# Optimization experiments

Measured on AMD Instinct MI355X. Metric: run time of the kernel, lower is better.

## Reference

```python
import jax, jax.numpy as jnp
import numpy as np
from jax import lax

N, L, D, P, H, QK, VP = 1, 512, 256, 128, 8, 8, 8
FIN = H * P + H * VP * 7 + H * 7  # 1528: pair + value-point + beta features


def _l2g(R, t, p):
    # local_to_global: q = R @ p + t, applied over flattened point dims
    s = p.shape
    p3 = p.reshape(s[0], s[1], -1, 3)
    q = jnp.einsum('nlij,nlmj->nlmi', R, p3) + t[:, :, None, :]
    return q.reshape(s)


def _g2l(R, t, q):
    # global_to_local: p = R^T @ (q - t)
    s = q.shape
    q3 = q.reshape(s[0], s[1], -1, 3)
    p = jnp.einsum('nlji,nlmj->nlmi', R, q3 - t[:, :, None, :])
    return p.reshape(s)


def _inorm(x):  # InstanceNorm2d, affine=False, eps=1e-5, NCHW
    m = x.mean(axis=(2, 3), keepdims=True)
    v = x.var(axis=(2, 3), keepdims=True)
    return (x - m) * lax.rsqrt(v + 1e-5)


def _conv3(x, w, b):  # 3x3, stride 1, pad 1
    y = lax.conv_general_dilated(x, w, (1, 1), [(1, 1), (1, 1)],
                                 dimension_numbers=('NCHW', 'OIHW', 'NCHW'))
    return y + b[None, :, None, None]


def _ln(x, g, b):  # LayerNorm over last dim, eps=1e-5
    m = x.mean(-1, keepdims=True)
    v = x.var(-1, keepdims=True)
    return (x - m) * lax.rsqrt(v + 1e-5) * g + b


def _leaky(x):  # LeakyReLU, negative_slope=0.01
    return jnp.where(x >= 0, x, 0.01 * x)


def setup_inputs():
    key = jax.random.key(0)
    ks = jax.random.split(key, 24)
    s = 0.05
    return {
        'R': jax.random.normal(ks[0], (N, L, 3, 3), jnp.float32),
        't': jax.random.normal(ks[1], (N, L, 3), jnp.float32),
        'p_CB': jax.random.normal(ks[2], (N, L, 3), jnp.float32),
        'x': jax.random.normal(ks[3], (N, L, D), jnp.float32),
        'z': jax.random.normal(ks[4], (N, L, L, P), jnp.float32),
        'W_p2h': jax.random.normal(ks[5], (P, H), jnp.float32) * s,
        'gamma': jnp.ones((1, 1, H), jnp.float32),
        'Wq': jax.random.normal(ks[6], (D, H * QK * 3), jnp.float32) * s,
        'Wk': jax.random.normal(ks[7], (D, H * QK * 3), jnp.float32) * s,
        'Wv': jax.random.normal(ks[8], (D, H * VP * 3), jnp.float32) * s,
        'W1': jax.random.normal(ks[9], (FIN, 2 * D), jnp.float32) * s,
        'b1': jnp.zeros((2 * D,), jnp.float32),
        'ln1_g': jnp.ones((2 * D,), jnp.float32),
        'ln1_b': jnp.zeros((2 * D,), jnp.float32),
        'W2': jax.random.normal(ks[10], (2 * D, D), jnp.float32) * s,
        'b2': jnp.zeros((D,), jnp.float32),
        'ca_w': jax.random.normal(ks[11], (H, 2 * H, 3, 3), jnp.float32) * s,
        'ca_b': jnp.zeros((H,), jnp.float32),
        'ln_g': jnp.ones((D,), jnp.float32),
        'ln_b': jnp.zeros((D,), jnp.float32),
        'cp_w': jax.random.normal(ks[12], (P, H + P, 3, 3), jnp.float32) * s,
        'cp_b': jnp.zeros((P,), jnp.float32),
        'mask': jnp.ones((N, L), dtype=bool),
    }


def reference(R, t, p_CB, x, z, W_p2h, gamma, Wq, Wk, Wv, W1, b1, ln1_g, ln1_b,
              W2, b2, ca_w, ca_b, ln_g, ln_b, cp_w, cp_b, mask):
    n, l = x.shape[:2]
    # pair logits [n,l,l,H]
    logits_pair = jnp.einsum('nijp,ph->nijh', z, W_p2h)
    # spatial (point) logits: squared distances between global q/k points
    q_s = _l2g(R, t, (x @ Wq).reshape(n, l, H * QK, 3)).reshape(n, l, H, QK * 3)
    k_s = _l2g(R, t, (x @ Wk).reshape(n, l, H * QK, 3)).reshape(n, l, H, QK * 3)
    ssd = ((q_s ** 2).sum(-1)[:, :, None, :] + (k_s ** 2).sum(-1)[:, None, :, :]
           - 2.0 * jnp.einsum('nihd,njhd->nijh', q_s, k_s))
    logits_spatial = ssd * (-gamma * jnp.sqrt(2.0 / (9.0 * QK)) / 2.0)
    # conv2dalpha: InstanceNorm -> 3x3 conv -> LeakyReLU over the LxL grid
    lg = jnp.concatenate([logits_pair, logits_spatial], axis=-1).transpose(0, 3, 1, 2)
    logits_sum = _leaky(_conv3(_inorm(lg), ca_w, ca_b)).transpose(0, 2, 3, 1)
    mask_row = mask[:, :, None, None]
    mask_pair = mask_row & mask[:, None, :, None]
    logits_sum = jnp.where(mask_pair, logits_sum, logits_sum - 1e6)
    alpha = jax.nn.softmax(logits_sum, axis=2)
    alpha = jnp.where(mask_row, alpha, 0.0)
    # pair aggregation [n,l,H*P]
    feat_p2n = jnp.einsum('nijh,nijp->nihp', alpha, z).reshape(n, l, H * P)
    # spatial (value point) aggregation
    v_pts = _l2g(R, t, (x @ Wv).reshape(n, l, H, VP, 3))
    aggr = jnp.einsum('nijh,njhvc->nihvc', alpha, v_pts)
    fp = _g2l(R, t, aggr)  # [n,l,H,VP,3]
    fn = jnp.sqrt((fp ** 2).sum(-1))
    fdir = fp / (fn[..., None] + 1e-6)
    feat_spatial = jnp.concatenate(
        [fp.reshape(n, l, -1), fn.reshape(n, l, -1), fdir.reshape(n, l, -1)], -1)
    # beta (CB point) aggregation
    aggr_b = jnp.einsum('nijh,njc->nihc', alpha, p_CB)
    fpb = _g2l(R, t, aggr_b)  # [n,l,H,3]
    fnb = jnp.sqrt((fpb ** 2).sum(-1))
    fdb = fpb / (fnb[..., None] + 1e-6)
    feat_beta = jnp.concatenate([fpb.reshape(n, l, -1), fnb, fdb.reshape(n, l, -1)], -1)
    # out_transform: Linear -> LayerNorm -> LeakyReLU -> Linear
    feat_all = jnp.concatenate([feat_p2n, feat_spatial, feat_beta], -1)
    h1 = _leaky(_ln(feat_all @ W1 + b1, ln1_g, ln1_b))
    fa = h1 @ W2 + b2
    fa = jnp.where(mask[..., None], fa, 0.0)
    x_out = _ln(x + fa, ln_g, ln_b)
    # alpha2pair: InstanceNorm -> 3x3 conv -> LeakyReLU
    pz = jnp.concatenate([z, alpha], -1).transpose(0, 3, 1, 2)
    pair_out = _leaky(_conv3(_inorm(pz), cp_w, cp_b)).transpose(0, 2, 3, 1)
    return (x_out, pair_out)
```

## Files before the change

kernel.cpp:

```cpp
#include <hip/hip_runtime.h>
#include <hip/hip_bf16.h>
#include <math.h>

#define Lr 512
#define LL (512*512)

typedef __bf16 bf16x8 __attribute__((ext_vector_type(8)));
typedef float f32x16 __attribute__((ext_vector_type(16)));

static __device__ __forceinline__ unsigned short f2bf(float f) {
    union { float f; unsigned u; } a; a.f = f;
    unsigned r = a.u + 0x7fff + ((a.u >> 16) & 1);
    return (unsigned short)(r >> 16);
}

__global__ __launch_bounds__(512) void zero_stats_k(float* lg_acc, float* pz_acc) {
    int t = threadIdx.x;
    if (t < 32) lg_acc[t] = 0.f;
    if (t < 272) pz_acc[t] = 0.f;
}

__global__ __launch_bounds__(256) void wb_prep_k(const float* __restrict__ cpw, unsigned short* __restrict__ wb) {
    int idx = blockIdx.x * 256 + threadIdx.x;
    if (idx >= 128 * 1296) return;
    int o = idx / 1296, k = idx % 1296;
    int tap = k / 144, c = k % 144;
    float v = (c < 136) ? cpw[(o * 136 + c) * 9 + tap] : 0.f;
    wb[idx] = f2bf(v);
}

__device__ __forceinline__ const float* qkv_colptr(const float* Wq, const float* Wk, const float* Wv, int c) {
    return c < 192 ? (Wq + c) : (c < 384 ? (Wk + c - 192) : (Wv + c - 384));
}

__global__ __launch_bounds__(256) void qkv_k(const float* __restrict__ x,
        const float* __restrict__ Wq, const float* __restrict__ Wk, const float* __restrict__ Wv,
        const float* __restrict__ R, const float* __restrict__ tv,
        float* __restrict__ qs, float* __restrict__ ks, float* __restrict__ vp,
        float* __restrict__ q2, float* __restrict__ k2) {
    __shared__ float xrow[256];
    __shared__ float praw[576];
    __shared__ float tr[576];
    __shared__ float Rt[12];
    int i = blockIdx.x, t = threadIdx.x;
    xrow[t] = x[i * 256 + t];
    if (t < 12) Rt[t] = (t < 9) ? R[i * 9 + t] : tv[i * 3 + t - 9];
    __syncthreads();
    const float* p0 = qkv_colptr(Wq, Wk, Wv, t);
    const float* p1 = qkv_colptr(Wq, Wk, Wv, t + 256);
    const float* p2 = qkv_colptr(Wq, Wk, Wv, t < 64 ? t + 512 : 575);
    float a0 = 0.f, a1 = 0.f, a2 = 0.f;
    for (int f = 0; f < 256; f++) {
        float xv = xrow[f];
        a0 += xv * p0[f * 192];
        a1 += xv * p1[f * 192];
        a2 += xv * p2[f * 192];
    }
    praw[t] = a0; praw[t + 256] = a1;
    if (t < 64) praw[t + 512] = a2;
    __syncthreads();
    if (t < 192) {
        int seg = t / 64, pt = t % 64;
        float b0 = praw[seg * 192 + pt * 3], b1_ = praw[seg * 192 + pt * 3 + 1], b2_ = praw[seg * 192 + pt * 3 + 2];
        #pragma unroll
        for (int r = 0; r < 3; r++)
            tr[seg * 192 + pt * 3 + r] = Rt[r * 3] * b0 + Rt[r * 3 + 1] * b1_ + Rt[r * 3 + 2] * b2_ + Rt[9 + r];
    }
    __syncthreads();
    if (t < 8) {
        float s = 0.f;
        #pragma unroll
        for (int d = 0; d < 24; d++) { float v = tr[t * 24 + d]; s += v * v; }
        q2[i * 8 + t] = s;
    } else if (t < 16) {
        int h = t - 8; float s = 0.f;
        #pragma unroll
        for (int d = 0; d < 24; d++) { float v = tr[192 + h * 24 + d]; s += v * v; }
        k2[i * 8 + h] = s;
    }
    for (int f = t; f < 576; f += 256) {
        float v = tr[f];
        if (f < 192) qs[i * 192 + f] = v;
        else if (f < 384) ks[i * 192 + f - 192] = v;
        else vp[i * 192 + f - 384] = v;
    }
}

__global__ __launch_bounds__(256) void zstats_k(const float4* __restrict__ z4, float* pz_acc) {
    __shared__ float acc[256];
    int t = threadIdx.x;
    acc[t] = 0.f;
    __syncthreads();
    float s[4] = {0,0,0,0}, s2[4] = {0,0,0,0};
    size_t base = (size_t)blockIdx.x * 4096;
    #pragma unroll
    for (int k = 0; k < 16; k++) {
        float4 v = z4[base + k * 256 + t];
        s[0] += v.x; s2[0] += v.x * v.x;
        s[1] += v.y; s2[1] += v.y * v.y;
        s[2] += v.z; s2[2] += v.z * v.z;
        s[3] += v.w; s2[3] += v.w * v.w;
    }
    int c0 = (4 * t) & 127;
    #pragma unroll
    for (int u = 0; u < 4; u++) {
        atomicAdd(&acc[(c0 + u) * 2], s[u]);
        atomicAdd(&acc[(c0 + u) * 2 + 1], s2[u]);
    }
    __syncthreads();
    if (t < 128) {
        atomicAdd(&pz_acc[t * 2], acc[t * 2]);
        atomicAdd(&pz_acc[t * 2 + 1], acc[t * 2 + 1]);
    }
}

__global__ __launch_bounds__(256) void lg_k(const float* __restrict__ z,
        const float* __restrict__ Wp2h, const float* __restrict__ gamma,
        const float* __restrict__ qs, const float* __restrict__ ks,
        const float* __restrict__ q2, const float* __restrict__ k2,
        float* __restrict__ lg, float* lg_acc) {
    __shared__ float zl[32 * 132];
    __shared__ float wh[8 * 132];
    __shared__ float qrow[192];
    __shared__ float q2row[8];
    __shared__ float sacc[32];
    int i = blockIdx.x, t = threadIdx.x;
    for (int f = t; f < 1024; f += 256) { int h = f >> 7, p = f & 127; wh[h * 132 + p] = Wp2h[p * 8 + h]; }
    if (t < 192) qrow[t] = qs[i * 192 + t];
    if (t < 8) q2row[t] = q2[i * 8 + t];
    if (t < 32) sacc[t] = 0.f;
    int jl = t >> 3, h = t & 7;
    float gsc = -gamma[h] * 0.08333333333333333f;
    float sp = 0.f, sp2 = 0.f, ss = 0.f, ss2 = 0.f;
    __syncthreads();
    for (int jt = 0; jt < 16; jt++) {
        int j0 = jt * 32;
        const float4* zsrc = (const float4*)(z + (size_t)(i * 512 + j0) * 128);
        #pragma unroll
        for (int r = 0; r < 4; r++) {
            int idx4 = r * 256 + t;
            int zjl = idx4 >> 5, p4 = idx4 & 31;
            *(float4*)&zl[zjl * 132 + p4 * 4] = zsrc[idx4];
        }
        __syncthreads();
        int j = j0 + jl;
        float accp = 0.f;
        const float4* za = (const float4*)&zl[jl * 132];
        const float4* wa = (const float4*)&wh[h * 132];
        #pragma unroll
        for (int p4 = 0; p4 < 32; p4++) {
            float4 a = za[p4], b = wa[p4];
            accp += a.x * b.x + a.y * b.y + a.z * b.z + a.w * b.w;
        }
        const float4* kp = (const float4*)(ks + (size_t)j * 192 + h * 24);
        const float4* qp = (const float4*)&qrow[h * 24];
        float dqk = 0.f;
        #pragma unroll
        for (int d4 = 0; d4 < 6; d4++) {
            float4 a = qp[d4], b = kp[d4];
            dqk += a.x * b.x + a.y * b.y + a.z * b.z + a.w * b.w;
        }
        float ssd = q2row[h] + k2[j * 8 + h] - 2.f * dqk;
        float lgs = ssd * gsc;
        lg[(size_t)h * LL + i * 512 + j] = accp;
        lg[(size_t)(8 + h) * LL + i * 512 + j] = lgs;
        sp += accp; sp2 += accp * accp; ss += lgs; ss2 += lgs * lgs;
        __syncthreads();
    }
    atomicAdd(&sacc[h * 2], sp);        atomicAdd(&sacc[h * 2 + 1], sp2);
    atomicAdd(&sacc[16 + h * 2], ss);   atomicAdd(&sacc[16 + h * 2 + 1], ss2);
    __syncthreads();
    if (t < 16) {
        atomicAdd(&lg_acc[t * 2], sacc[t * 2]);
        atomicAdd(&lg_acc[t * 2 + 1], sacc[t * 2 + 1]);
    }
}

__global__ void finalize_k(const float* __restrict__ acc, float* __restrict__ mr, int nch, float npix) {
    int t = threadIdx.x;
    if (t < nch) {
        float m = acc[t * 2] / npix;
        float v = acc[t * 2 + 1] / npix - m * m;
        mr[t * 2] = m;
        mr[t * 2 + 1] = rsqrtf(fmaxf(v, 0.f) + 1e-5f);
    }
}

__global__ __launch_bounds__(256) void ca_softmax_k(const float* __restrict__ lg,
        const float* __restrict__ lgmr, const float* __restrict__ caw, const float* __restrict__ cab,
        float* __restrict__ alpha, float* pz_acc) {
    __shared__ float wl[1152];
    __shared__ float mr[32];
    __shared__ float cb[8];
    __shared__ float red[64];
    int i = blockIdx.x, t = threadIdx.x;
    for (int f = t; f < 1152; f += 256) {
        int o = f & 7, k = f >> 3; int c = k / 9, r = k % 9;
        wl[f] = caw[(o * 16 + c) * 9 + r];
    }
    if (t < 32) mr[t] = lgmr[t];
    if (t < 8) cb[t] = cab[t];
    __syncthreads();
    float acc0[8], acc1[8];
    #pragma unroll
    for (int o = 0; o < 8; o++) { acc0[o] = 0.f; acc1[o] = 0.f; }
    int j0 = t, j1 = t + 256;
    const float4* w4 = (const float4*)wl;
    for (int c = 0; c < 16; c++) {
        float m = mr[c * 2], rs = mr[c * 2 + 1];
        const float* lgc = lg + (size_t)c * LL;
        #pragma unroll
        for (int di = 0; di < 3; di++) {
            int row = i - 1 + di;
            if (row < 0 || row >= 512) continue;
            const float* lr = lgc + (size_t)row * 512;
            float v0[3], v1[3];
            v0[0] = (j0 > 0) ? (lr[j0 - 1] - m) * rs : 0.f;
            v0[1] = (lr[j0] - m) * rs;
            v0[2] = (lr[j0 + 1] - m) * rs;
            v1[0] = (lr[j1 - 1] - m) * rs;
            v1[1] = (lr[j1] - m) * rs;
            v1[2] = (j1 < 511) ? (lr[j1 + 1] - m) * rs : 0.f;
            int wb = (c * 9 + di * 3) * 2;
            #pragma unroll
            for (int dj = 0; dj < 3; dj++) {
                float4 wa = w4[wb + dj * 2], wbv = w4[wb + dj * 2 + 1];
                acc0[0] += wa.x * v0[dj]; acc0[1] += wa.y * v0[dj]; acc0[2] += wa.z * v0[dj]; acc0[3] += wa.w * v0[dj];
                acc0[4] += wbv.x * v0[dj]; acc0[5] += wbv.y * v0[dj]; acc0[6] += wbv.z * v0[dj]; acc0[7] += wbv.w * v0[dj];
                acc1[0] += wa.x * v1[dj]; acc1[1] += wa.y * v1[dj]; acc1[2] += wa.z * v1[dj]; acc1[3] += wa.w * v1[dj];
                acc1[4] += wbv.x * v1[dj]; acc1[5] += wbv.y * v1[dj]; acc1[6] += wbv.z * v1[dj]; acc1[7] += wbv.w * v1[dj];
            }
        }
    }
    float s0[8], s1[8];
    #pragma unroll
    for (int o = 0; o < 8; o++) {
        float v = acc0[o] + cb[o]; s0[o] = v >= 0.f ? v : 0.01f * v;
        float w = acc1[o] + cb[o]; s1[o] = w >= 0.f ? w : 0.01f * w;
    }
    int lane = t & 63, wid = t >> 6;
    float mx[8];
    #pragma unroll
    for (int o = 0; o < 8; o++) mx[o] = fmaxf(s0[o], s1[o]);
    for (int off = 1; off < 64; off <<= 1) {
        #pragma unroll
        for (int o = 0; o < 8; o++) mx[o] = fmaxf(mx[o], __shfl_xor(mx[o], off));
    }
    if (lane == 0) {
        #pragma unroll
        for (int o = 0; o < 8; o++) red[wid * 8 + o] = mx[o];
    }
    __syncthreads();
    float M[8];
    #pragma unroll
    for (int o = 0; o < 8; o++) M[o] = fmaxf(fmaxf(red[o], red[8 + o]), fmaxf(red[16 + o], red[24 + o]));
    float e0[8], e1[8], sm[8];
    #pragma unroll
    for (int o = 0; o < 8; o++) { e0[o] = expf(s0[o] - M[o]); e1[o] = expf(s1[o] - M[o]); sm[o] = e0[o] + e1[o]; }
    __syncthreads();
    for (int off = 1; off < 64; off <<= 1) {
        #pragma unroll
        for (int o = 0; o < 8; o++) sm[o] += __shfl_xor(sm[o], off);
    }
    if (lane == 0) {
        #pragma unroll
        for (int o = 0; o < 8; o++) red[wid * 8 + o] = sm[o];
    }
    __syncthreads();
    float a0[8], a1[8], st_s[8], st_q[8];
    #pragma unroll
    for (int o = 0; o < 8; o++) {
        float rden = 1.f / (red[o] + red[8 + o] + red[16 + o] + red[24 + o]);
        a0[o] = e0[o] * rden; a1[o] = e1[o] * rden;
        st_s[o] = a0[o] + a1[o];
        st_q[o] = a0[o] * a0[o] + a1[o] * a1[o];
    }
    size_t base = (size_t)i * 512;
    #pragma unroll
    for (int o = 0; o < 8; o++) {
        alpha[(size_t)o * LL + base + t] = a0[o];
        alpha[(size_t)o * LL + base + t + 256] = a1[o];
    }
    __syncthreads();
    for (int off = 1; off < 64; off <<= 1) {
        #pragma unroll
        for (int o = 0; o < 8; o++) { st_s[o] += __shfl_xor(st_s[o], off); st_q[o] += __shfl_xor(st_q[o], off); }
    }
    if (lane == 0) {
        #pragma unroll
        for (int o = 0; o < 8; o++) { red[wid * 8 + o] = st_s[o]; red[32 + wid * 8 + o] = st_q[o]; }
    }
    __syncthreads();
    if (t < 8) {
        float ts = red[t] + red[8 + t] + red[16 + t] + red[24 + t];
        float tq = red[32 + t] + red[40 + t] + red[48 + t] + red[56 + t];
        atomicAdd(&pz_acc[(128 + t) * 2], ts);
        atomicAdd(&pz_acc[(128 + t) * 2 + 1], tq);
    }
}

__global__ __launch_bounds__(256) void feat_mlp_k(
        const float* __restrict__ alpha, const float* __restrict__ z,
        const float* __restrict__ vp, const float* __restrict__ pcb,
        const float* __restrict__ R, const float* __restrict__ tv,
        const float* __restrict__ W1, const float* __restrict__ b1,
        const float* __restrict__ ln1g, const float* __restrict__ ln1b,
        const float* __restrict__ W2, const float* __restrict__ b2,
        const float* __restrict__ lng, const float* __restrict__ lnb,
        const float* __restrict__ x, float* __restrict__ xout) {
    __shared__ float al[8 * 512];
    __shared__ float zl[64 * 128];
    __shared__ float feat[1536];
    __shared__ float h1[512];
    __shared__ float agg[216];
    __shared__ float Rt[12];
    __shared__ float redl[8];
    int i = blockIdx.x, t = threadIdx.x;
    for (int f = t; f < 4096; f += 256) al[f] = alpha[(size_t)(f >> 9) * LL + i * 512 + (f & 511)];
    if (t < 12) Rt[t] = (t < 9) ? R[i * 9 + t] : tv[i * 3 + t - 9];
    __syncthreads();
    if (t < 216) {
        float a = 0.f;
        if (t < 192) {
            int h = t / 24;
            const float* vptr = vp + t;
            const float* ar = al + h * 512;
            for (int j = 0; j < 512; j++) a += ar[j] * vptr[(size_t)j * 192];
        } else {
            int u = t - 192; int h = u / 3, cc = u % 3;
            const float* ar = al + h * 512;
            for (int j = 0; j < 512; j++) a += ar[j] * pcb[j * 3 + cc];
        }
        agg[t] = a;
    }
    float4 accp = {0.f, 0.f, 0.f, 0.f};
    int hh = t >> 5, p4 = t & 31;
    for (int jc = 0; jc < 8; jc++) {
        const float4* zsrc = (const float4*)(z + (size_t)(i * 512 + jc * 64) * 128);
        #pragma unroll
        for (int r = 0; r < 8; r++) ((float4*)zl)[r * 256 + t] = zsrc[r * 256 + t];
        __syncthreads();
        const float* ar = al + hh * 512 + jc * 64;
        const float4* zv = (const float4*)zl + p4;
        #pragma unroll 4
        for (int jl = 0; jl < 64; jl++) {
            float a = ar[jl];
            float4 v = zv[jl * 32];
            accp.x += a * v.x; accp.y += a * v.y; accp.z += a * v.z; accp.w += a * v.w;
        }
        __syncthreads();
    }
    *(float4*)&feat[hh * 128 + p4 * 4] = accp;
    __syncthreads();
    if (t < 64) {
        int h = t >> 3, v = t & 7;
        float d0 = agg[h * 24 + v * 3] - Rt[9];
        float d1 = agg[h * 24 + v * 3 + 1] - Rt[10];
        float d2 = agg[h * 24 + v * 3 + 2] - Rt[11];
        float f0 = Rt[0] * d0 + Rt[3] * d1 + Rt[6] * d2;
        float f1 = Rt[1] * d0 + Rt[4] * d1 + Rt[7] * d2;
        float f2 = Rt[2] * d0 + Rt[5] * d1 + Rt[8] * d2;
        float n = sqrtf(f0 * f0 + f1 * f1 + f2 * f2);
        float rn = 1.f / (n + 1e-6f);
        feat[1024 + h * 24 + v * 3] = f0;
        feat[1024 + h * 24 + v * 3 + 1] = f1;
        feat[1024 + h * 24 + v * 3 + 2] = f2;
        feat[1216 + h * 8 + v] = n;
        feat[1280 + h * 24 + v * 3] = f0 * rn;
        feat[1280 + h * 24 + v * 3 + 1] = f1 * rn;
        feat[1280 + h * 24 + v * 3 + 2] = f2 * rn;
    } else if (t < 72) {
        int h = t - 64;
        float d0 = agg[192 + h * 3] - Rt[9];
        float d1 = agg[192 + h * 3 + 1] - Rt[10];
        float d2 = agg[192 + h * 3 + 2] - Rt[11];
        float f0 = Rt[0] * d0 + Rt[3] * d1 + Rt[6] * d2;
        float f1 = Rt[1] * d0 + Rt[4] * d1 + Rt[7] * d2;
        float f2 = Rt[2] * d0 + Rt[5] * d1 + Rt[8] * d2;
        float n = sqrtf(f0 * f0 + f1 * f1 + f2 * f2);
        float rn = 1.f / (n + 1e-6f);
        feat[1472 + h * 3] = f0; feat[1472 + h * 3 + 1] = f1; feat[1472 + h * 3 + 2] = f2;
        feat[1496 + h] = n;
        feat[1504 + h * 3] = f0 * rn; feat[1504 + h * 3 + 1] = f1 * rn; feat[1504 + h * 3 + 2] = f2 * rn;
    }
    __syncthreads();
    float acc0 = b1[t], acc1 = b1[t + 256];
    const float4* f4 = (const float4*)feat;
    for (int f = 0; f < 1528; f += 4) {
        float4 fv = f4[f >> 2];
        const float* w = W1 + (size_t)f * 512 + t;
        acc0 += fv.x * w[0] + fv.y * w[512] + fv.z * w[1024] + fv.w * w[1536];
        const float* w2p = w + 256;
        acc1 += fv.x * w2p[0] + fv.y * w2p[512] + fv.z * w2p[1024] + fv.w * w2p[1536];
    }
    int lane = t & 63, wid = t >> 6;
    float s = acc0 + acc1, s2 = acc0 * acc0 + acc1 * acc1;
    for (int off = 1; off < 64; off <<= 1) { s += __shfl_xor(s, off); s2 += __shfl_xor(s2, off); }
    if (lane == 0) { redl[wid * 2] = s; redl[wid * 2 + 1] = s2; }
    __syncthreads();
    float S = redl[0] + redl[2] + redl[4] + redl[6];
    float S2 = redl[1] + redl[3] + redl[5] + redl[7];
    float mean = S / 512.f;
    float rstd = rsqrtf(fmaxf(S2 / 512.f - mean * mean, 0.f) + 1e-5f);
    float hv0 = (acc0 - mean) * rstd * ln1g[t] + ln1b[t];
    float hv1 = (acc1 - mean) * rstd * ln1g[t + 256] + ln1b[t + 256];
    hv0 = hv0 >= 0.f ? hv0 : 0.01f * hv0;
    hv1 = hv1 >= 0.f ? hv1 : 0.01f * hv1;
    h1[t] = hv0; h1[t + 256] = hv1;
    __syncthreads();
    float a2 = b2[t];
    const float4* h14 = (const float4*)h1;
    for (int k = 0; k < 512; k += 4) {
        float4 hv = h14[k >> 2];
        const float* w = W2 + (size_t)k * 256 + t;
        a2 += hv.x * w[0] + hv.y * w[256] + hv.z * w[512] + hv.w * w[768];
    }
    float xv = x[i * 256 + t] + a2;
    float ss_ = xv, sq_ = xv * xv;
    for (int off = 1; off < 64; off <<= 1) { ss_ += __shfl_xor(ss_, off); sq_ += __shfl_xor(sq_, off); }
    __syncthreads();
    if (lane == 0) { redl[wid * 2] = ss_; redl[wid * 2 + 1] = sq_; }
    __syncthreads();
    float Sx = redl[0] + redl[2] + redl[4] + redl[6];
    float Sx2 = redl[1] + redl[3] + redl[5] + redl[7];
    float mx = Sx / 256.f;
    float rsx = rsqrtf(fmaxf(Sx2 / 256.f - mx * mx, 0.f) + 1e-5f);
    xout[i * 256 + t] = (xv - mx) * rsx * lng[t] + lnb[t];
}

__global__ __launch_bounds__(256) void conv_mfma_k(
        const float* __restrict__ z, const float* __restrict__ alpha,
        const float* __restrict__ pzmr, const unsigned short* __restrict__ wb,
        const float* __restrict__ cpb, float* __restrict__ pout) {
    __shared__ unsigned short rowbuf[130 * 144];
    __shared__ float mr[272];
    int t = threadIdx.x;
    int i  = blockIdx.x >> 2;
    int j0 = (blockIdx.x & 3) * 128;
    for (int f = t; f < 272; f += 256) mr[f] = pzmr[f];
    int w = t >> 6, lane = t & 63;
    int l31 = lane & 31, lhi = lane >> 5;
    int mt0 = (w & 1) * 64;
    int nt0 = (w >> 1) * 64;
    f32x16 acc00 = {}, acc01 = {}, acc10 = {}, acc11 = {};
    for (int di = 0; di < 3; di++) {
        int grow = i - 1 + di;
        bool rowok = (grow >= 0 && grow < 512);
        __syncthreads();
        for (int f4 = t; f4 < 130 * 34; f4 += 256) {
            int col = f4 / 34, c4 = (f4 % 34) * 4;
            int gcol = j0 - 1 + col;
            float4 v = {0.f, 0.f, 0.f, 0.f};
            if (rowok && gcol >= 0 && gcol < 512) {
                int sp = grow * 512 + gcol;
                if (c4 < 128) {
                    v = ((const float4*)z)[(size_t)sp * 32 + (c4 >> 2)];
                } else {
                    int h0 = c4 - 128;
                    v.x = alpha[(size_t)h0 * LL + sp];
                    v.y = alpha[(size_t)(h0 + 1) * LL + sp];
                    v.z = alpha[(size_t)(h0 + 2) * LL + sp];
                    v.w = alpha[(size_t)(h0 + 3) * LL + sp];
                }
                v.x = (v.x - mr[c4 * 2])     * mr[c4 * 2 + 1];
                v.y = (v.y - mr[c4 * 2 + 2]) * mr[c4 * 2 + 3];
                v.z = (v.z - mr[c4 * 2 + 4]) * mr[c4 * 2 + 5];
                v.w = (v.w - mr[c4 * 2 + 6]) * mr[c4 * 2 + 7];
            }
            ushort4 pk;
            pk.x = f2bf(v.x); pk.y = f2bf(v.y); pk.z = f2bf(v.z); pk.w = f2bf(v.w);
            *(ushort4*)&rowbuf[col * 144 + c4] = pk;
        }
        for (int f = t; f < 130 * 2; f += 256) {
            int col = f >> 1, g = f & 1;
            ushort4 zr = {0, 0, 0, 0};
            *(ushort4*)&rowbuf[col * 144 + 136 + g * 4] = zr;
        }
        __syncthreads();
        #pragma unroll
        for (int dj = 0; dj < 3; dj++) {
            int tap = di * 3 + dj;
            const unsigned short* wp0 = wb + (size_t)(nt0 + l31) * 1296 + tap * 144 + lhi * 8;
            const unsigned short* wp1 = wp0 + 32 * 1296;
            const unsigned short* ap0 = &rowbuf[(mt0 + l31 + dj) * 144 + lhi * 8];
            const unsigned short* ap1 = ap0 + 32 * 144;
            #pragma unroll
            for (int ks = 0; ks < 9; ks++) {
                bf16x8 a0 = *(const bf16x8*)(ap0 + ks * 16);
                bf16x8 a1 = *(const bf16x8*)(ap1 + ks * 16);
                bf16x8 b0 = *(const bf16x8*)(wp0 + ks * 16);
                bf16x8 b1 = *(const bf16x8*)(wp1 + ks * 16);
                acc00 = __builtin_amdgcn_mfma_f32_32x32x16_bf16(a0, b0, acc00, 0, 0, 0);
                acc01 = __builtin_amdgcn_mfma_f32_32x32x16_bf16(a0, b1, acc01, 0, 0, 0);
                acc10 = __builtin_amdgcn_mfma_f32_32x32x16_bf16(a1, b0, acc10, 0, 0, 0);
                acc11 = __builtin_amdgcn_mfma_f32_32x32x16_bf16(a1, b1, acc11, 0, 0, 0);
            }
        }
    }
    #pragma unroll
    for (int mi = 0; mi < 2; mi++) {
        #pragma unroll
        for (int ni = 0; ni < 2; ni++) {
            const f32x16* a = (mi == 0) ? (ni == 0 ? &acc00 : &acc01) : (ni == 0 ? &acc10 : &acc11);
            int nb = nt0 + ni * 32 + l31;
            float bias = cpb[nb];
            #pragma unroll
            for (int r = 0; r < 16; r++) {
                int m = mt0 + mi * 32 + 4 * lhi + (r & 3) + 8 * (r >> 2);
                float v = (*a)[r] + bias;
                v = v >= 0.f ? v : 0.01f * v;
                pout[((size_t)(i * 512 + j0 + m)) * 128 + nb] = v;
            }
        }
    }
}

extern "C" void kernel_launch(void* const* d_in, const int* in_sizes, int n_in,
                              void* d_out, int out_size, void* d_ws, size_t ws_size,
                              hipStream_t stream) {
    (void)in_sizes; (void)n_in; (void)out_size; (void)ws_size;
    const float* R    = (const float*)d_in[0];
    const float* tv   = (const float*)d_in[1];
    const float* pcb  = (const float*)d_in[2];
    const float* x    = (const float*)d_in[3];
    const float* z    = (const float*)d_in[4];
    const float* wp2h = (const float*)d_in[5];
    const float* gamma= (const float*)d_in[6];
    const float* Wq   = (const float*)d_in[7];
    const float* Wk   = (const float*)d_in[8];
    const float* Wv   = (const float*)d_in[9];
    const float* W1   = (const float*)d_in[10];
    const float* b1   = (const float*)d_in[11];
    const float* ln1g = (const float*)d_in[12];
    const float* ln1b = (const float*)d_in[13];
    const float* W2   = (const float*)d_in[14];
    const float* b2   = (const float*)d_in[15];
    const float* caw  = (const float*)d_in[16];
    const float* cab  = (const float*)d_in[17];
    const float* lng  = (const float*)d_in[18];
    const float* lnb  = (const float*)d_in[19];
    const float* cpw  = (const float*)d_in[20];
    const float* cpb  = (const float*)d_in[21];

    float* ws = (float*)d_ws;
    float* qs     = ws;
    float* ks     = qs + 98304;
    float* vp     = ks + 98304;
    float* q2     = vp + 98304;
    float* k2     = q2 + 4096;
    float* lg_acc = k2 + 4096;
    float* lg_mr  = lg_acc + 32;
    float* pz_acc = lg_mr + 32;
    float* pz_mr  = pz_acc + 272;
    unsigned short* wbq = (unsigned short*)(pz_mr + 272);
    float* lg     = pz_mr + 272 + 82944;
    float* alpha  = lg + 16 * LL;

    float* xout = (float*)d_out;
    float* pout = xout + 131072;

    hipLaunchKernelGGL(zero_stats_k, dim3(1), dim3(512), 0, stream, lg_acc, pz_acc);
    hipLaunchKernelGGL(wb_prep_k, dim3(648), dim3(256), 0, stream, cpw, wbq);
    hipLaunchKernelGGL(qkv_k, dim3(512), dim3(256), 0, stream, x, Wq, Wk, Wv, R, tv, qs, ks, vp, q2, k2);
    hipLaunchKernelGGL(zstats_k, dim3(2048), dim3(256), 0, stream, (const float4*)z, pz_acc);
    hipLaunchKernelGGL(lg_k, dim3(512), dim3(256), 0, stream, z, wp2h, gamma, qs, ks, q2, k2, lg, lg_acc);
    hipLaunchKernelGGL(finalize_k, dim3(1), dim3(64), 0, stream, lg_acc, lg_mr, 16, 262144.f);
    hipLaunchKernelGGL(ca_softmax_k, dim3(512), dim3(256), 0, stream, lg, lg_mr, caw, cab, alpha, pz_acc);
    hipLaunchKernelGGL(finalize_k, dim3(1), dim3(192), 0, stream, pz_acc, pz_mr, 136, 262144.f);
    hipLaunchKernelGGL(feat_mlp_k, dim3(512), dim3(256), 0, stream,
                       alpha, z, vp, pcb, R, tv, W1, b1, ln1g, ln1b, W2, b2, lng, lnb, x, xout);
    hipLaunchKernelGGL(conv_mfma_k, dim3(2048), dim3(256), 0, stream, z, alpha, pz_mr, wbq, cpb, pout);
}
```

Baseline: 799.0 us.

## Fold instance-norm into conv weights and pre-pack pair input as bf16

The instance-norm scale is folded into the bf16 conv weights. The mean shift becomes a per-output, per-tap bias correction, with explicit handling of image borders where zero padding drops taps. The z statistics pass and the softmax kernel now also write a pre-normalized bf16 copy of z and alpha in a channel-chunked layout. This lets the conv kernel load tiles with plain 16-byte copies instead of reading fp32 z/alpha, normalizing and converting on every 3x3 row reload. It also swizzles block order, and it adds an extra bf16 buffer write, a changed rounding point (raw values rather than normalized ones are quantized), and more workspace.

Result: faster. 782.1 us (-2.1%).

```diff
diff --git a/kernel.cpp b/kernel.cpp
--- a/kernel.cpp
+++ b/kernel.cpp
@@ -4,6 +4,7 @@
 
 #define Lr 512
 #define LL (512*512)
+#define PZROW 73728
 
 typedef __bf16 bf16x8 __attribute__((ext_vector_type(8)));
 typedef float f32x16 __attribute__((ext_vector_type(16)));
@@ -14,19 +15,35 @@
     return (unsigned short)(r >> 16);
 }
 
+static __device__ __forceinline__ unsigned pack2(float lo, float hi) {
+    return (unsigned)f2bf(lo) | ((unsigned)f2bf(hi) << 16);
+}
+
 __global__ __launch_bounds__(512) void zero_stats_k(float* lg_acc, float* pz_acc) {
     int t = threadIdx.x;
     if (t < 32) lg_acc[t] = 0.f;
     if (t < 272) pz_acc[t] = 0.f;
 }
 
-__global__ __launch_bounds__(256) void wb_prep_k(const float* __restrict__ cpw, unsigned short* __restrict__ wb) {
+__global__ __launch_bounds__(256) void wb_prep_k(const float* __restrict__ cpw,
+        const float* __restrict__ pzmr, unsigned short* __restrict__ wb) {
     int idx = blockIdx.x * 256 + threadIdx.x;
     if (idx >= 128 * 1296) return;
     int o = idx / 1296, k = idx % 1296;
     int tap = k / 144, c = k % 144;
-    float v = (c < 136) ? cpw[(o * 136 + c) * 9 + tap] : 0.f;
+    float v = (c < 136) ? cpw[(o * 136 + c) * 9 + tap] * pzmr[c * 2 + 1] : 0.f;
     wb[idx] = f2bf(v);
+}
+
+__global__ __launch_bounds__(128) void kc_prep_k(const float* __restrict__ cpw,
+        const float* __restrict__ pzmr, float* __restrict__ kc) {
+    int idx = blockIdx.x * 128 + threadIdx.x;
+    if (idx >= 1152) return;
+    int o = idx / 9, tap = idx % 9;
+    float s = 0.f;
+    for (int c = 0; c < 136; c++)
+        s += cpw[(o * 136 + c) * 9 + tap] * pzmr[c * 2 + 1] * pzmr[c * 2];
+    kc[idx] = -s;
 }
 
 __device__ __forceinline__ const float* qkv_colptr(const float* Wq, const float* Wk, const float* Wv, int c) {
@@ -86,26 +103,35 @@
     }
 }
 
-__global__ __launch_bounds__(256) void zstats_k(const float4* __restrict__ z4, float* pz_acc) {
+__global__ __launch_bounds__(256) void zstats_pzb_k(const float4* __restrict__ z4,
+        float* pz_acc, unsigned short* __restrict__ pzb) {
     __shared__ float acc[256];
     int t = threadIdx.x;
     acc[t] = 0.f;
     __syncthreads();
-    float s[4] = {0,0,0,0}, s2[4] = {0,0,0,0};
-    size_t base = (size_t)blockIdx.x * 4096;
-    #pragma unroll
-    for (int k = 0; k < 16; k++) {
-        float4 v = z4[base + k * 256 + t];
-        s[0] += v.x; s2[0] += v.x * v.x;
-        s[1] += v.y; s2[1] += v.y * v.y;
-        s[2] += v.z; s2[2] += v.z * v.z;
-        s[3] += v.w; s2[3] += v.w * v.w;
-    }
-    int c0 = (4 * t) & 127;
-    #pragma unroll
-    for (int u = 0; u < 4; u++) {
-        atomicAdd(&acc[(c0 + u) * 2], s[u]);
-        atomicAdd(&acc[(c0 + u) * 2 + 1], s2[u]);
+    int chunk = t & 15, pl = t >> 4;
+    int p0 = blockIdx.x * 128;
+    float s[8], s2[8];
+    #pragma unroll
+    for (int u = 0; u < 8; u++) { s[u] = 0.f; s2[u] = 0.f; }
+    #pragma unroll
+    for (int k = 0; k < 8; k++) {
+        int pos = p0 + k * 16 + pl;
+        const float4* src = z4 + (size_t)pos * 32 + chunk * 2;
+        float4 v0 = src[0], v1 = src[1];
+        float vv[8] = {v0.x, v0.y, v0.z, v0.w, v1.x, v1.y, v1.z, v1.w};
+        #pragma unroll
+        for (int u = 0; u < 8; u++) { s[u] += vv[u]; s2[u] += vv[u] * vv[u]; }
+        uint4 q;
+        q.x = pack2(vv[0], vv[1]); q.y = pack2(vv[2], vv[3]);
+        q.z = pack2(vv[4], vv[5]); q.w = pack2(vv[6], vv[7]);
+        int row = pos >> 9, col = pos & 511;
+        *(uint4*)(pzb + ((size_t)row * 18 + chunk) * 4096 + col * 8) = q;
+    }
+    #pragma unroll
+    for (int u = 0; u < 8; u++) {
+        atomicAdd(&acc[(chunk * 8 + u) * 2], s[u]);
+        atomicAdd(&acc[(chunk * 8 + u) * 2 + 1], s2[u]);
     }
     __syncthreads();
     if (t < 128) {
@@ -188,7 +214,7 @@
 
 __global__ __launch_bounds__(256) void ca_softmax_k(const float* __restrict__ lg,
         const float* __restrict__ lgmr, const float* __restrict__ caw, const float* __restrict__ cab,
-        float* __restrict__ alpha, float* pz_acc) {
+        float* __restrict__ alpha, float* pz_acc, unsigned short* __restrict__ pzb) {
     __shared__ float wl[1152];
     __shared__ float mr[32];
     __shared__ float cb[8];
@@ -280,6 +306,19 @@
     for (int o = 0; o < 8; o++) {
         alpha[(size_t)o * LL + base + t] = a0[o];
         alpha[(size_t)o * LL + base + t + 256] = a1[o];
+    }
+    {
+        uint4 p0, p1;
+        p0.x = pack2(a0[0], a0[1]); p0.y = pack2(a0[2], a0[3]);
+        p0.z = pack2(a0[4], a0[5]); p0.w = pack2(a0[6], a0[7]);
+        p1.x = pack2(a1[0], a1[1]); p1.y = pack2(a1[2], a1[3]);
+        p1.z = pack2(a1[4], a1[5]); p1.w = pack2(a1[6], a1[7]);
+        unsigned short* pb = pzb + (size_t)i * PZROW + 16 * 4096;
+        *(uint4*)(pb + (size_t)t * 8) = p0;
+        *(uint4*)(pb + (size_t)(t + 256) * 8) = p1;
+        uint4 zz = {0u, 0u, 0u, 0u};
+        *(uint4*)(pb + 4096 + (size_t)t * 8) = zz;
+        *(uint4*)(pb + 4096 + (size_t)(t + 256) * 8) = zz;
     }
     __syncthreads();
     for (int off = 1; off < 64; off <<= 1) {
@@ -429,15 +468,31 @@
 }
 
 __global__ __launch_bounds__(256) void conv_mfma_k(
-        const float* __restrict__ z, const float* __restrict__ alpha,
-        const float* __restrict__ pzmr, const unsigned short* __restrict__ wb,
-        const float* __restrict__ cpb, float* __restrict__ pout) {
-    __shared__ unsigned short rowbuf[130 * 144];
-    __shared__ float mr[272];
+        const unsigned short* __restrict__ pzb, const unsigned short* __restrict__ wb,
+        const float* __restrict__ kc, const float* __restrict__ cpb,
+        float* __restrict__ pout) {
+    __shared__ unsigned short abuf[2368 * 8];
+    __shared__ float csA[128];
+    __shared__ float cs0[128];
+    __shared__ float cs2[128];
     int t = threadIdx.x;
-    int i  = blockIdx.x >> 2;
-    int j0 = (blockIdx.x & 3) * 128;
-    for (int f = t; f < 272; f += 256) mr[f] = pzmr[f];
+    int bid = blockIdx.x;
+    int swz = (bid & 7) * 256 + (bid >> 3);
+    int i = swz >> 2;
+    int j0 = (swz & 3) * 128;
+    if (t < 128) {
+        int o = t;
+        float a0 = 0.f, a1 = 0.f, a2 = 0.f;
+        #pragma unroll
+        for (int di = 0; di < 3; di++) {
+            int grow = i - 1 + di;
+            if (grow < 0 || grow > 511) continue;
+            a0 += kc[o * 9 + di * 3];
+            a1 += kc[o * 9 + di * 3 + 1];
+            a2 += kc[o * 9 + di * 3 + 2];
+        }
+        cs0[o] = a0; cs2[o] = a2; csA[o] = cpb[o] + a0 + a1 + a2;
+    }
     int w = t >> 6, lane = t & 63;
     int l31 = lane & 31, lhi = lane >> 5;
     int mt0 = (w & 1) * 64;
@@ -447,34 +502,15 @@
         int grow = i - 1 + di;
         bool rowok = (grow >= 0 && grow < 512);
         __syncthreads();
-        for (int f4 = t; f4 < 130 * 34; f4 += 256) {
-            int col = f4 / 34, c4 = (f4 % 34) * 4;
+        const unsigned short* rowp = pzb + (size_t)grow * PZROW;
+        for (int f = t; f < 2340; f += 256) {
+            int c = f / 130;
+            int col = f - c * 130;
             int gcol = j0 - 1 + col;
-            float4 v = {0.f, 0.f, 0.f, 0.f};
-            if (rowok && gcol >= 0 && gcol < 512) {
-                int sp = grow * 512 + gcol;
-                if (c4 < 128) {
-                    v = ((const float4*)z)[(size_t)sp * 32 + (c4 >> 2)];
-                } else {
-                    int h0 = c4 - 128;
-                    v.x = alpha[(size_t)h0 * LL + sp];
-                    v.y = alpha[(size_t)(h0 + 1) * LL + sp];
-                    v.z = alpha[(size_t)(h0 + 2) * LL + sp];
-                    v.w = alpha[(size_t)(h0 + 3) * LL + sp];
-                }
-                v.x = (v.x - mr[c4 * 2])     * mr[c4 * 2 + 1];
-                v.y = (v.y - mr[c4 * 2 + 2]) * mr[c4 * 2 + 3];
-                v.z = (v.z - mr[c4 * 2 + 4]) * mr[c4 * 2 + 5];
-                v.w = (v.w - mr[c4 * 2 + 6]) * mr[c4 * 2 + 7];
-            }
-            ushort4 pk;
-            pk.x = f2bf(v.x); pk.y = f2bf(v.y); pk.z = f2bf(v.z); pk.w = f2bf(v.w);
-            *(ushort4*)&rowbuf[col * 144 + c4] = pk;
-        }
-        for (int f = t; f < 130 * 2; f += 256) {
-            int col = f >> 1, g = f & 1;
-            ushort4 zr = {0, 0, 0, 0};
-            *(ushort4*)&rowbuf[col * 144 + 136 + g * 4] = zr;
+            uint4 v = {0u, 0u, 0u, 0u};
+            if (rowok && (unsigned)gcol < 512u)
+                v = *(const uint4*)(rowp + c * 4096 + gcol * 8);
+            *(uint4*)(abuf + f * 8) = v;
         }
         __syncthreads();
         #pragma unroll
@@ -482,14 +518,14 @@
             int tap = di * 3 + dj;
             const unsigned short* wp0 = wb + (size_t)(nt0 + l31) * 1296 + tap * 144 + lhi * 8;
             const unsigned short* wp1 = wp0 + 32 * 1296;
-            const unsigned short* ap0 = &rowbuf[(mt0 + l31 + dj) * 144 + lhi * 8];
-            const unsigned short* ap1 = ap0 + 32 * 144;
+            const unsigned short* ap0 = abuf + lhi * 1040 + (mt0 + l31 + dj) * 8;
+            const unsigned short* ap1 = ap0 + 256;
             #pragma unroll
-            for (int ks = 0; ks < 9; ks++) {
-                bf16x8 a0 = *(const bf16x8*)(ap0 + ks * 16);
-                bf16x8 a1 = *(const bf16x8*)(ap1 + ks * 16);
-                bf16x8 b0 = *(const bf16x8*)(wp0 + ks * 16);
-                bf16x8 b1 = *(const bf16x8*)(wp1 + ks * 16);
+            for (int ksn = 0; ksn < 9; ksn++) {
+                bf16x8 a0 = *(const bf16x8*)(ap0 + ksn * 2080);
+                bf16x8 a1 = *(const bf16x8*)(ap1 + ksn * 2080);
+                bf16x8 b0 = *(const bf16x8*)(wp0 + ksn * 16);
+                bf16x8 b1 = *(const bf16x8*)(wp1 + ksn * 16);
                 acc00 = __builtin_amdgcn_mfma_f32_32x32x16_bf16(a0, b0, acc00, 0, 0, 0);
                 acc01 = __builtin_amdgcn_mfma_f32_32x32x16_bf16(a0, b1, acc01, 0, 0, 0);
                 acc10 = __builtin_amdgcn_mfma_f32_32x32x16_bf16(a1, b0, acc10, 0, 0, 0);
@@ -503,13 +539,15 @@
         for (int ni = 0; ni < 2; ni++) {
             const f32x16* a = (mi == 0) ? (ni == 0 ? &acc00 : &acc01) : (ni == 0 ? &acc10 : &acc11);
             int nb = nt0 + ni * 32 + l31;
-            float bias = cpb[nb];
+            float bA = csA[nb], b0_ = cs0[nb], b2_ = cs2[nb];
             #pragma unroll
             for (int r = 0; r < 16; r++) {
                 int m = mt0 + mi * 32 + 4 * lhi + (r & 3) + 8 * (r >> 2);
+                int j = j0 + m;
+                float bias = bA - (j == 0 ? b0_ : 0.f) - (j == 511 ? b2_ : 0.f);
                 float v = (*a)[r] + bias;
                 v = v >= 0.f ? v : 0.01f * v;
-                pout[((size_t)(i * 512 + j0 + m)) * 128 + nb] = v;
+                pout[((size_t)(i * 512 + j)) * 128 + nb] = v;
             }
         }
     }
@@ -544,30 +582,33 @@
 
     float* ws = (float*)d_ws;
     float* qs     = ws;
-    float* ks     = qs + 98304;
-    float* vp     = ks + 98304;
+    float* ksv    = qs + 98304;
+    float* vp     = ksv + 98304;
     float* q2     = vp + 98304;
     float* k2     = q2 + 4096;
     float* lg_acc = k2 + 4096;
     float* lg_mr  = lg_acc + 32;
     float* pz_acc = lg_mr + 32;
     float* pz_mr  = pz_acc + 272;
-    unsigned short* wbq = (unsigned short*)(pz_mr + 272);
-    float* lg     = pz_mr + 272 + 82944;
+    float* kc     = pz_mr + 272;
+    unsigned short* wbq = (unsigned short*)(kc + 1152);
+    float* lg     = kc + 1152 + 82944;
     float* alpha  = lg + 16 * LL;
+    unsigned short* pzb = (unsigned short*)(alpha + 8 * LL);
 
     float* xout = (float*)d_out;
     float* pout = xout + 131072;
 
     hipLaunchKernelGGL(zero_stats_k, dim3(1), dim3(512), 0, stream, lg_acc, pz_acc);
-    hipLaunchKernelGGL(wb_prep_k, dim3(648), dim3(256), 0, stream, cpw, wbq);
-    hipLaunchKernelGGL(qkv_k, dim3(512), dim3(256), 0, stream, x, Wq, Wk, Wv, R, tv, qs, ks, vp, q2, k2);
-    hipLaunchKernelGGL(zstats_k, dim3(2048), dim3(256), 0, stream, (const float4*)z, pz_acc);
-    hipLaunchKernelGGL(lg_k, dim3(512), dim3(256), 0, stream, z, wp2h, gamma, qs, ks, q2, k2, lg, lg_acc);
+    hipLaunchKernelGGL(qkv_k, dim3(512), dim3(256), 0, stream, x, Wq, Wk, Wv, R, tv, qs, ksv, vp, q2, k2);
+    hipLaunchKernelGGL(zstats_pzb_k, dim3(2048), dim3(256), 0, stream, (const float4*)z, pz_acc, pzb);
+    hipLaunchKernelGGL(lg_k, dim3(512), dim3(256), 0, stream, z, wp2h, gamma, qs, ksv, q2, k2, lg, lg_acc);
     hipLaunchKernelGGL(finalize_k, dim3(1), dim3(64), 0, stream, lg_acc, lg_mr, 16, 262144.f);
-    hipLaunchKernelGGL(ca_softmax_k, dim3(512), dim3(256), 0, stream, lg, lg_mr, caw, cab, alpha, pz_acc);
+    hipLaunchKernelGGL(ca_softmax_k, dim3(512), dim3(256), 0, stream, lg, lg_mr, caw, cab, alpha, pz_acc, pzb);
     hipLaunchKernelGGL(finalize_k, dim3(1), dim3(192), 0, stream, pz_acc, pz_mr, 136, 262144.f);
+    hipLaunchKernelGGL(wb_prep_k, dim3(648), dim3(256), 0, stream, cpw, pz_mr, wbq);
+    hipLaunchKernelGGL(kc_prep_k, dim3(9), dim3(128), 0, stream, cpw, pz_mr, kc);
     hipLaunchKernelGGL(feat_mlp_k, dim3(512), dim3(256), 0, stream,
                        alpha, z, vp, pcb, R, tv, W1, b1, ln1g, ln1b, W2, b2, lng, lnb, x, xout);
-    hipLaunchKernelGGL(conv_mfma_k, dim3(2048), dim3(256), 0, stream, z, alpha, pz_mr, wbq, cpb, pout);
-}
+    hipLaunchKernelGGL(conv_mfma_k, dim3(2048), dim3(256), 0, stream, pzb, wbq, kc, cpb, pout);
+}
```
